# Performance work log

Measured on AMD Instinct MI355X. Metric: run time of the kernel, lower is better.

Reference implementation:

```python
import jax, jax.numpy as jnp
import numpy as np

N_TREES = 100
N_TRAIN = 40000
N_QUERY = 1024
N_LEAVES = 512
EPS = 1e-8


def setup_inputs() -> dict:
    key = jax.random.key(0)
    k1, k2 = jax.random.split(key)
    # Per-tree leaf id of each query point: equivalent of tree.apply(X) per tree.
    query_leaf_ids = jax.random.randint(k1, (N_TREES, N_QUERY), 0, N_LEAVES, dtype=jnp.int32)
    # Per-tree leaf id of each training point: equivalent of tree.apply(X_train).
    train_leaf_ids = jax.random.randint(k2, (N_TREES, N_TRAIN), 0, N_LEAVES, dtype=jnp.int32)
    # Uniform vote weight per tree (original sums unit counts then divides by T).
    tree_weights = jnp.ones((N_TREES,), dtype=jnp.float32)
    return {
        "tree_weights": tree_weights,
        "query_leaf_ids": query_leaf_ids,
        "train_leaf_ids": train_leaf_ids,
    }


def reference(tree_weights, query_leaf_ids, train_leaf_ids):
    # weights[m, j] = (1/T) * sum_t tw[t] * 1[leaf_t(query m) == leaf_t(train j)]
    T = tree_weights.shape[0]
    M = query_leaf_ids.shape[1]
    n_train = train_leaf_ids.shape[1]

    def step(acc, inputs):
        tw, q_leaf, tr_leaf = inputs  # scalar, [M], [n_train]
        # Co-membership indicator for this tree: [M, n_train]
        ind = (q_leaf[:, None] == tr_leaf[None, :]).astype(acc.dtype)
        return acc + tw * ind, None

    init = jnp.zeros((M, n_train), dtype=jnp.float32)
    weights, _ = jax.lax.scan(step, init, (tree_weights, query_leaf_ids, train_leaf_ids))
    weights = weights / T  # average over trees
    # Row-normalize so each query's weights sum to 1 (with eps, as in original).
    weights = weights / (jnp.sum(weights, axis=1, keepdims=True) + EPS)
    return weights
```

## Files before the change

kernel.cpp:

```cpp
#include <hip/hip_runtime.h>
#include <hip/hip_bf16.h>
#include <stdint.h>

#define N_TREES  100
#define N_TRAIN  40000
#define N_QUERY  1024
#define N_LEAVES 512
#define QTRAIN   (N_TRAIN / 4)
#define PADTRAIN 44096

#define BIDX_BYTES ((size_t)N_TREES * PADTRAIN * 2)
#define BPK_OFF    BIDX_BYTES
#define BPK_BYTES  ((size_t)N_TREES * N_LEAVES * 4)
#define WS_NEEDED  (BPK_OFF + BPK_BYTES)

__global__ __launch_bounds__(1024) void build(const int* __restrict__ train,
                                              uint32_t* __restrict__ bpk,
                                              uint16_t* __restrict__ bidx) {
    const int t   = blockIdx.x;
    const int tid = threadIdx.x;
    __shared__ __align__(16) uint16_t sorted[PADTRAIN];
    __shared__ uint32_t hist[N_LEAVES];
    __shared__ uint32_t sbuf[2][N_LEAVES];
    __shared__ uint32_t cursor[N_LEAVES];
    __shared__ uint32_t totpad_sh;

    if (tid < N_LEAVES) hist[tid] = 0;
    __syncthreads();

    const int4* tr4 = (const int4*)(train + t * N_TRAIN);
    for (int i = tid; i < N_TRAIN / 4; i += 1024) {
        int4 v = tr4[i];
        atomicAdd(&hist[v.x], 1u);
        atomicAdd(&hist[v.y], 1u);
        atomicAdd(&hist[v.z], 1u);
        atomicAdd(&hist[v.w], 1u);
    }
    __syncthreads();

    uint32_t len = 0, lp = 0;
    if (tid < N_LEAVES) {
        len = hist[tid];
        lp  = (len + 7u) & ~7u;
        sbuf[0][tid] = lp;
    }
    __syncthreads();
    int src = 0;
    for (int d = 1; d < N_LEAVES; d <<= 1) {
        if (tid < N_LEAVES) {
            uint32_t v = sbuf[src][tid];
            if (tid >= d) v += sbuf[src][tid - d];
            sbuf[src ^ 1][tid] = v;
        }
        __syncthreads();
        src ^= 1;
    }
    if (tid < N_LEAVES) {
        uint32_t start = sbuf[src][tid] - lp;
        bpk[t * N_LEAVES + tid] = (len << 16) | start;
        cursor[tid] = start;
        if (tid == N_LEAVES - 1) totpad_sh = sbuf[src][N_LEAVES - 1];
    }
    __syncthreads();

    for (int i = tid; i < N_TRAIN / 4; i += 1024) {
        int4 v = tr4[i];
        int  j = i * 4;
        uint32_t p0 = atomicAdd(&cursor[v.x], 1u); sorted[p0] = (uint16_t)j;
        uint32_t p1 = atomicAdd(&cursor[v.y], 1u); sorted[p1] = (uint16_t)(j + 1);
        uint32_t p2 = atomicAdd(&cursor[v.z], 1u); sorted[p2] = (uint16_t)(j + 2);
        uint32_t p3 = atomicAdd(&cursor[v.w], 1u); sorted[p3] = (uint16_t)(j + 3);
    }
    __syncthreads();

    const uint32_t n16 = (totpad_sh + 7u) >> 3;
    const uint4* s4 = (const uint4*)sorted;
    uint4* g4 = (uint4*)(bidx + (size_t)t * PADTRAIN);
    for (uint32_t i = tid; i < n16; i += 1024) g4[i] = s4[i];
}

__global__ __launch_bounds__(512) void row_kernel(const int* __restrict__ qleaf,
                                                  const uint16_t* __restrict__ bidx,
                                                  const uint32_t* __restrict__ bpk,
                                                  float* __restrict__ out) {
    const int m   = blockIdx.x;
    const int tid = threadIdx.x;
    __shared__ __align__(16) uint32_t cnt[QTRAIN];
    __shared__ uint16_t su[N_TREES];
    __shared__ uint16_t lu[N_TREES];
    __shared__ uint16_t cpref[N_TREES + 4];
    __shared__ float    inv_sh;

    uint4* c4 = (uint4*)cnt;
    for (int i = tid; i < QTRAIN / 4; i += 512) c4[i] = make_uint4(0, 0, 0, 0);
    if (tid < N_TREES) {
        int q = qleaf[tid * N_QUERY + m];
        uint32_t pk = bpk[tid * N_LEAVES + q];
        su[tid] = (uint16_t)(pk & 0xffffu);
        lu[tid] = (uint16_t)(pk >> 16);
    }
    __syncthreads();

    if (tid < 64) {
        int i0 = 2 * tid, i1 = 2 * tid + 1;
        uint32_t l0 = (i0 < N_TREES) ? lu[i0] : 0u;
        uint32_t l1 = (i1 < N_TREES) ? lu[i1] : 0u;
        uint32_t c0 = (l0 + 7u) >> 3, c1 = (l1 + 7u) >> 3;
        uint32_t s   = c0 + c1;
        uint32_t inc = s;
        for (int o = 1; o < 64; o <<= 1) {
            uint32_t v = __shfl_up(inc, o, 64);
            if (tid >= o) inc += v;
        }
        uint32_t excl = inc - s;
        if (i0 < N_TREES) cpref[i0] = (uint16_t)excl;
        if (i1 < N_TREES) cpref[i1] = (uint16_t)(excl + c0);
        if (tid == 63) cpref[N_TREES] = (uint16_t)inc;
        uint32_t tot = l0 + l1;
        for (int o = 32; o > 0; o >>= 1) tot += __shfl_down(tot, o, 64);
        if (tid == 0) inv_sh = 1.0f / ((float)tot + 1e-6f);
    }
    __syncthreads();

    const int Ctot = cpref[N_TREES];
    for (int c = tid; c < Ctot; c += 512) {
        int t = 0;
        #pragma unroll
        for (int step = 64; step >= 1; step >>= 1) {
            int cand = t + step;
            if (cand <= N_TREES - 1 && (int)cpref[cand] <= c) t = cand;
        }
        const int cc  = c - (int)cpref[t];
        const int rem = (int)lu[t] - cc * 8;
        const int n   = rem > 8 ? 8 : rem;
        const uint4 w = *(const uint4*)(bidx + (size_t)t * PADTRAIN + su[t] + cc * 8);
        uint32_t e[8] = { w.x & 0xffffu, w.x >> 16, w.y & 0xffffu, w.y >> 16,
                          w.z & 0xffffu, w.z >> 16, w.w & 0xffffu, w.w >> 16 };
        #pragma unroll
        for (int i = 0; i < 8; ++i)
            if (i < n) {
                uint32_t j = e[i];
                atomicAdd(&cnt[j >> 2], 1u << ((j & 3u) * 8u));
            }
    }
    __syncthreads();

    const float inv = inv_sh;
    float4* orow = (float4*)(out + (size_t)m * N_TRAIN);
    for (int p = tid * 2; p < QTRAIN; p += 1024) {
        uint32_t w0 = cnt[p], w1 = cnt[p + 1];
        float4 a, b;
        a.x = (float)(w0 & 0xffu) * inv;
        a.y = (float)((w0 >> 8) & 0xffu) * inv;
        a.z = (float)((w0 >> 16) & 0xffu) * inv;
        a.w = (float)(w0 >> 24) * inv;
        b.x = (float)(w1 & 0xffu) * inv;
        b.y = (float)((w1 >> 8) & 0xffu) * inv;
        b.z = (float)((w1 >> 16) & 0xffu) * inv;
        b.w = (float)(w1 >> 24) * inv;
        orow[p]     = a;
        orow[p + 1] = b;
    }
}

__global__ __launch_bounds__(1024) void row_kernel_direct(const int* __restrict__ qleaf,
                                                          const int* __restrict__ train,
                                                          float* __restrict__ out) {
    const int m   = blockIdx.x;
    const int tid = threadIdx.x;
    __shared__ uint32_t cnt[N_TRAIN / 2];
    __shared__ int      qlds[N_TREES];
    __shared__ uint32_t total_sh;

    if (tid < N_TREES) qlds[tid] = qleaf[tid * N_QUERY + m];
    if (tid == 0) total_sh = 0;
    __syncthreads();

    const int2* tr2 = (const int2*)train;
    for (int p = tid; p < N_TRAIN / 2; p += 1024) {
        uint32_t c0 = 0, c1 = 0;
        for (int t = 0; t < N_TREES; ++t) {
            const int q = qlds[t];
            int2 v = tr2[t * (N_TRAIN / 2) + p];
            c0 += (v.x == q);
            c1 += (v.y == q);
        }
        cnt[p] = c0 | (c1 << 16);
    }
    __syncthreads();

    uint32_t local = 0;
    for (int p = tid; p < N_TRAIN / 2; p += 1024) {
        uint32_t w = cnt[p];
        local += (w & 0xffffu) + (w >> 16);
    }
    const int lane = tid & 63;
    for (int o = 32; o > 0; o >>= 1) local += __shfl_down(local, o, 64);
    if (lane == 0) atomicAdd(&total_sh, local);
    __syncthreads();

    const float inv = 1.0f / ((float)total_sh + 1e-6f);
    float2* orow = (float2*)(out + (size_t)m * N_TRAIN);
    for (int p = tid; p < N_TRAIN / 2; p += 1024) {
        uint32_t w = cnt[p];
        float2 v;
        v.x = (float)(w & 0xffffu) * inv;
        v.y = (float)(w >> 16) * inv;
        orow[p] = v;
    }
}

extern "C" void kernel_launch(void* const* d_in, const int* in_sizes, int n_in,
                              void* d_out, int out_size, void* d_ws, size_t ws_size,
                              hipStream_t stream) {
    const int* qleaf = (const int*)d_in[1];
    const int* train = (const int*)d_in[2];
    float* out = (float*)d_out;

    if (ws_size >= WS_NEEDED) {
        uint16_t* bidx = (uint16_t*)d_ws;
        uint32_t* bpk  = (uint32_t*)((char*)d_ws + BPK_OFF);
        build<<<N_TREES, 1024, 0, stream>>>(train, bpk, bidx);
        row_kernel<<<N_QUERY, 512, 0, stream>>>(qleaf, bidx, bpk, out);
    } else {
        row_kernel_direct<<<N_QUERY, 1024, 0, stream>>>(qleaf, train, out);
    }
}
```

Before: 52.46 us.

## Split bucket build across two blocks per tree, batch gathers, nontemporal stores

The build kernel now launches two 512-thread blocks per tree, each scattering only half of the leaves into a smaller shared staging buffer, with an overflow path that writes directly to global memory. This doubles the number of blocks and cuts shared memory per block to raise occupancy, at the cost of each block re-reading the tree's training ids and recomputing the full histogram. The row kernel issues two chunk gathers per thread before applying the atomics, to overlap global load latency. Output rows are written with nontemporal stores to avoid polluting the cache.

```diff
diff --git a/kernel.cpp b/kernel.cpp
--- a/kernel.cpp
+++ b/kernel.cpp
@@ -8,28 +8,34 @@
 #define N_LEAVES 512
 #define QTRAIN   (N_TRAIN / 4)
 #define PADTRAIN 44096
+#define HALF_LEAVES 256
+#define STAGE_CAP   24576
+
+typedef float f32x4 __attribute__((ext_vector_type(4)));
 
 #define BIDX_BYTES ((size_t)N_TREES * PADTRAIN * 2)
 #define BPK_OFF    BIDX_BYTES
 #define BPK_BYTES  ((size_t)N_TREES * N_LEAVES * 4)
 #define WS_NEEDED  (BPK_OFF + BPK_BYTES)
 
-__global__ __launch_bounds__(1024) void build(const int* __restrict__ train,
-                                              uint32_t* __restrict__ bpk,
-                                              uint16_t* __restrict__ bidx) {
-    const int t   = blockIdx.x;
-    const int tid = threadIdx.x;
-    __shared__ __align__(16) uint16_t sorted[PADTRAIN];
+__global__ __launch_bounds__(512) void build(const int* __restrict__ train,
+                                             uint32_t* __restrict__ bpk,
+                                             uint16_t* __restrict__ bidx) {
+    const int t    = blockIdx.x >> 1;
+    const int half = blockIdx.x & 1;
+    const int base = half * HALF_LEAVES;
+    const int tid  = threadIdx.x;
+    __shared__ __align__(16) uint16_t stage[STAGE_CAP];
     __shared__ uint32_t hist[N_LEAVES];
     __shared__ uint32_t sbuf[2][N_LEAVES];
-    __shared__ uint32_t cursor[N_LEAVES];
-    __shared__ uint32_t totpad_sh;
-
-    if (tid < N_LEAVES) hist[tid] = 0;
+    __shared__ uint32_t cursor[HALF_LEAVES];
+    __shared__ uint32_t sbase_sh, span_sh;
+
+    hist[tid] = 0;
     __syncthreads();
 
     const int4* tr4 = (const int4*)(train + t * N_TRAIN);
-    for (int i = tid; i < N_TRAIN / 4; i += 1024) {
+    for (int i = tid; i < N_TRAIN / 4; i += 512) {
         int4 v = tr4[i];
         atomicAdd(&hist[v.x], 1u);
         atomicAdd(&hist[v.y], 1u);
@@ -38,45 +44,74 @@
     }
     __syncthreads();
 
-    uint32_t len = 0, lp = 0;
-    if (tid < N_LEAVES) {
-        len = hist[tid];
-        lp  = (len + 7u) & ~7u;
-        sbuf[0][tid] = lp;
-    }
+    const uint32_t len = hist[tid];
+    const uint32_t lp  = (len + 7u) & ~7u;
+    sbuf[0][tid] = lp;
     __syncthreads();
     int src = 0;
     for (int d = 1; d < N_LEAVES; d <<= 1) {
-        if (tid < N_LEAVES) {
-            uint32_t v = sbuf[src][tid];
-            if (tid >= d) v += sbuf[src][tid - d];
-            sbuf[src ^ 1][tid] = v;
-        }
+        uint32_t v = sbuf[src][tid];
+        if (tid >= d) v += sbuf[src][tid - d];
+        sbuf[src ^ 1][tid] = v;
         __syncthreads();
         src ^= 1;
     }
-    if (tid < N_LEAVES) {
-        uint32_t start = sbuf[src][tid] - lp;
+    const uint32_t start = sbuf[src][tid] - lp;
+    if (tid >= base && tid < base + HALF_LEAVES) {
         bpk[t * N_LEAVES + tid] = (len << 16) | start;
-        cursor[tid] = start;
-        if (tid == N_LEAVES - 1) totpad_sh = sbuf[src][N_LEAVES - 1];
-    }
-    __syncthreads();
-
-    for (int i = tid; i < N_TRAIN / 4; i += 1024) {
+        cursor[tid - base] = start;
+    }
+    if (tid == 0) {
+        sbase_sh = (base == 0) ? 0u : sbuf[src][base - 1];
+        span_sh  = sbuf[src][base + HALF_LEAVES - 1];
+    }
+    __syncthreads();
+
+    const uint32_t sbase = sbase_sh;
+    uint16_t* bo = bidx + (size_t)t * PADTRAIN;
+
+    for (int i = tid; i < N_TRAIN / 4; i += 512) {
         int4 v = tr4[i];
         int  j = i * 4;
-        uint32_t p0 = atomicAdd(&cursor[v.x], 1u); sorted[p0] = (uint16_t)j;
-        uint32_t p1 = atomicAdd(&cursor[v.y], 1u); sorted[p1] = (uint16_t)(j + 1);
-        uint32_t p2 = atomicAdd(&cursor[v.z], 1u); sorted[p2] = (uint16_t)(j + 2);
-        uint32_t p3 = atomicAdd(&cursor[v.w], 1u); sorted[p3] = (uint16_t)(j + 3);
-    }
-    __syncthreads();
-
-    const uint32_t n16 = (totpad_sh + 7u) >> 3;
-    const uint4* s4 = (const uint4*)sorted;
-    uint4* g4 = (uint4*)(bidx + (size_t)t * PADTRAIN);
-    for (uint32_t i = tid; i < n16; i += 1024) g4[i] = s4[i];
+        #pragma unroll
+        for (int s = 0; s < 4; ++s) {
+            int leaf = (s == 0) ? v.x : (s == 1) ? v.y : (s == 2) ? v.z : v.w;
+            if ((unsigned)(leaf - base) < (unsigned)HALF_LEAVES) {
+                uint32_t pos = atomicAdd(&cursor[leaf - base], 1u);
+                uint32_t rel = pos - sbase;
+                if (rel < STAGE_CAP) stage[rel] = (uint16_t)(j + s);
+                else                 bo[pos]    = (uint16_t)(j + s);
+            }
+        }
+    }
+    __syncthreads();
+
+    uint32_t span = span_sh - sbase;
+    if (span > STAGE_CAP) span = STAGE_CAP;
+    const uint4* s4 = (const uint4*)stage;
+    uint4* g4 = (uint4*)(bo + sbase);
+    for (uint32_t i = tid; i < (span >> 3); i += 512) g4[i] = s4[i];
+}
+
+__device__ __forceinline__ int find_tree(const uint16_t* cpref, int c) {
+    int t = 0;
+    #pragma unroll
+    for (int step = 64; step >= 1; step >>= 1) {
+        int cand = t + step;
+        if (cand <= N_TREES - 1 && (int)cpref[cand] <= c) t = cand;
+    }
+    return t;
+}
+
+__device__ __forceinline__ void apply_chunk(uint32_t* cnt, uint4 w, int n) {
+    uint32_t e[8] = { w.x & 0xffffu, w.x >> 16, w.y & 0xffffu, w.y >> 16,
+                      w.z & 0xffffu, w.z >> 16, w.w & 0xffffu, w.w >> 16 };
+    #pragma unroll
+    for (int i = 0; i < 8; ++i)
+        if (i < n) {
+            uint32_t j = e[i];
+            atomicAdd(&cnt[j >> 2], 1u << ((j & 3u) * 8u));
+        }
 }
 
 __global__ __launch_bounds__(512) void row_kernel(const int* __restrict__ qleaf,
@@ -123,33 +158,31 @@
     __syncthreads();
 
     const int Ctot = cpref[N_TREES];
-    for (int c = tid; c < Ctot; c += 512) {
-        int t = 0;
-        #pragma unroll
-        for (int step = 64; step >= 1; step >>= 1) {
-            int cand = t + step;
-            if (cand <= N_TREES - 1 && (int)cpref[cand] <= c) t = cand;
-        }
-        const int cc  = c - (int)cpref[t];
-        const int rem = (int)lu[t] - cc * 8;
-        const int n   = rem > 8 ? 8 : rem;
-        const uint4 w = *(const uint4*)(bidx + (size_t)t * PADTRAIN + su[t] + cc * 8);
-        uint32_t e[8] = { w.x & 0xffffu, w.x >> 16, w.y & 0xffffu, w.y >> 16,
-                          w.z & 0xffffu, w.z >> 16, w.w & 0xffffu, w.w >> 16 };
-        #pragma unroll
-        for (int i = 0; i < 8; ++i)
-            if (i < n) {
-                uint32_t j = e[i];
-                atomicAdd(&cnt[j >> 2], 1u << ((j & 3u) * 8u));
-            }
+    for (int c = tid; c < Ctot; c += 1024) {
+        const int tA  = find_tree(cpref, c);
+        const int ccA = c - (int)cpref[tA];
+        const uint4 wA = *(const uint4*)(bidx + (size_t)tA * PADTRAIN + su[tA] + ccA * 8);
+        const int nA  = min((int)lu[tA] - ccA * 8, 8);
+
+        const int cB = c + 512;
+        const bool hasB = cB < Ctot;
+        uint4 wB; int nB = 0;
+        if (hasB) {
+            const int tB  = find_tree(cpref, cB);
+            const int ccB = cB - (int)cpref[tB];
+            wB = *(const uint4*)(bidx + (size_t)tB * PADTRAIN + su[tB] + ccB * 8);
+            nB = min((int)lu[tB] - ccB * 8, 8);
+        }
+        apply_chunk(cnt, wA, nA);
+        if (hasB) apply_chunk(cnt, wB, nB);
     }
     __syncthreads();
 
     const float inv = inv_sh;
-    float4* orow = (float4*)(out + (size_t)m * N_TRAIN);
+    f32x4* orow = (f32x4*)(out + (size_t)m * N_TRAIN);
     for (int p = tid * 2; p < QTRAIN; p += 1024) {
         uint32_t w0 = cnt[p], w1 = cnt[p + 1];
-        float4 a, b;
+        f32x4 a, b;
         a.x = (float)(w0 & 0xffu) * inv;
         a.y = (float)((w0 >> 8) & 0xffu) * inv;
         a.z = (float)((w0 >> 16) & 0xffu) * inv;
@@ -158,8 +191,8 @@
         b.y = (float)((w1 >> 8) & 0xffu) * inv;
         b.z = (float)((w1 >> 16) & 0xffu) * inv;
         b.w = (float)(w1 >> 24) * inv;
-        orow[p]     = a;
-        orow[p + 1] = b;
+        __builtin_nontemporal_store(a, &orow[p]);
+        __builtin_nontemporal_store(b, &orow[p + 1]);
     }
 }
 
@@ -220,7 +253,7 @@
     if (ws_size >= WS_NEEDED) {
         uint16_t* bidx = (uint16_t*)d_ws;
         uint32_t* bpk  = (uint32_t*)((char*)d_ws + BPK_OFF);
-        build<<<N_TREES, 1024, 0, stream>>>(train, bpk, bidx);
+        build<<<N_TREES * 2, 512, 0, stream>>>(train, bpk, bidx);
         row_kernel<<<N_QUERY, 512, 0, stream>>>(qleaf, bidx, bpk, out);
     } else {
         row_kernel_direct<<<N_QUERY, 1024, 0, stream>>>(qleaf, train, out);
```

New measurement: 97.00 us. 1.85x slower.
